# Optimization experiments

Measured on AMD Instinct MI355X. Metric: run time of the kernel, lower is better.

The kernel has to match this reference:

```python
import jax, jax.numpy as jnp
import numpy as np

B, S, F, H = 64, 1024, 64, 128


def setup_inputs() -> dict:
    key = jax.random.key(0)
    ks = jax.random.split(key, 12)
    s = 1.0 / np.sqrt(H)
    u = lambda k, shape: jax.random.uniform(k, shape, jnp.float32, -s, s)
    return {
        "x": jax.random.normal(ks[0], (B, S, F), jnp.float32),
        "mu": jax.random.normal(ks[1], (B, 1, F), jnp.float32),
        "W_ih0": u(ks[2], (4 * H, F)),
        "W_hh0": u(ks[3], (4 * H, H)),
        "b_ih0": u(ks[4], (4 * H,)),
        "b_hh0": u(ks[5], (4 * H,)),
        "W_ih1": u(ks[6], (4 * H, H)),
        "W_hh1": u(ks[7], (4 * H, H)),
        "b_ih1": u(ks[8], (4 * H,)),
        "b_hh1": u(ks[9], (4 * H,)),
        "fc_w": u(ks[10], (1, H)),
        "fc_b": u(ks[11], (1,)),
    }


def _cell(x_gates, h, c, Whh, bias):
    # PyTorch LSTM cell: gates ordered i, f, g, o
    g = x_gates + h @ Whh.T + bias
    i, f, gg, o = jnp.split(g, 4, axis=-1)
    c = jax.nn.sigmoid(f) * c + jax.nn.sigmoid(i) * jnp.tanh(gg)
    h = jax.nn.sigmoid(o) * jnp.tanh(c)
    return h, c


def _lstm2(x1, x2, Wih, Whh, bih, bhh):
    # 2-step LSTM layer from zero initial state; returns per-step hidden states
    bias = bih + bhh
    n = x1.shape[0]
    hd = Whh.shape[1]
    h0 = jnp.zeros((n, hd), x1.dtype)
    h1, c1 = _cell(x1 @ Wih.T, h0, h0, Whh, bias)
    h2, _ = _cell(x2 @ Wih.T, h1, c1, Whh, bias)
    return h1, h2


def reference(x, mu, W_ih0, W_hh0, b_ih0, b_hh0, W_ih1, W_hh1, b_ih1, b_hh1, fc_w, fc_b):
    b, s, f = x.shape
    # Every timestep runs an independent 2-step LSTM [x_t, mu] from zero state,
    # so fold (batch, seq) into one big batch of B*S instances.
    x1 = x.reshape(b * s, f)                                   # step-1 inputs
    x2 = jnp.broadcast_to(mu, (b, s, f)).reshape(b * s, f)     # step-2 inputs (mu)
    h1, h2 = _lstm2(x1, x2, W_ih0, W_hh0, b_ih0, b_hh0)        # layer 0
    _, h2 = _lstm2(h1, h2, W_ih1, W_hh1, b_ih1, b_hh1)         # layer 1
    h = jax.nn.relu(h2).reshape(b, s, -1)                      # relu; dropout is identity (eval)
    out = h @ fc_w.T + fc_b                                    # [B, S, 1]
    return out
```

## Files before the change

### kernel.cpp

```cpp
#include <hip/hip_runtime.h>


typedef _Float16 half8 __attribute__((ext_vector_type(8)));
typedef _Float16 half4_t __attribute__((ext_vector_type(4)));
typedef float f32x4 __attribute__((ext_vector_type(4)));

#define L2E  1.4426950408889634f
#define L2E2 2.8853900817779268f

#define WP_WIH0 0
#define WP_WHH0 32768
#define WP_WIH1 98304
#define WP_WHH1 163840
#define WS_BIAS0 458752
#define WS_BIAS1 (458752 + 2048)
#define WS_MUG2  (458752 + 4096)

__global__ void prep_kernel(const float* __restrict__ Wih0,
                            const float* __restrict__ Whh0,
                            const float* __restrict__ Wih1,
                            const float* __restrict__ Whh1,
                            const float* __restrict__ bih0,
                            const float* __restrict__ bhh0,
                            const float* __restrict__ bih1,
                            const float* __restrict__ bhh1,
                            const float* __restrict__ mu,
                            _Float16* __restrict__ Wp,
                            float* __restrict__ bias0f,
                            float* __restrict__ bias1f,
                            float* __restrict__ mu_g2)
{
    int blk = blockIdx.x;
    if (blk >= 113) {
        int o = (blk - 113) * 256 + threadIdx.x;
        int b = o >> 9;
        int n = o & 511;
        float s = bih0[n] + bhh0[n];
        const float* m = mu + b * 64;
        const float* wrow = Wih0 + n * 64;
        #pragma unroll 8
        for (int k = 0; k < 64; ++k) s += m[k] * wrow[k];
        float scale = ((n >> 7) == 2) ? L2E2 : L2E;
        mu_g2[o] = s * scale;
        return;
    }
    if (blk == 112) {
        int i = threadIdx.x;
        float sc_hi = (i < 128) ? L2E2 : L2E;
        bias0f[i]       = (bih0[i]       + bhh0[i])       * L2E;
        bias0f[i + 256] = (bih0[i + 256] + bhh0[i + 256]) * sc_hi;
        bias1f[i]       = (bih1[i]       + bhh1[i])       * L2E;
        bias1f[i + 256] = (bih1[i + 256] + bhh1[i + 256]) * sc_hi;
        return;
    }
    int gidx = blk * 256 + threadIdx.x;
    const float* src; int KC, Kw, local;
    if (gidx < 4096)       { src = Wih0; KC = 2; Kw = 64;  local = gidx; }
    else if (gidx < 12288) { src = Whh0; KC = 4; Kw = 128; local = gidx - 4096; }
    else if (gidx < 20480) { src = Wih1; KC = 4; Kw = 128; local = gidx - 12288; }
    else                   { src = Whh1; KC = 4; Kw = 128; local = gidx - 20480; }
    int lane = local & 63;
    int tmp  = local >> 6;
    int kc   = tmp % KC;
    int nt   = tmp / KC;
    int n  = nt * 16 + (lane & 15);
    int k0 = kc * 32 + (lane >> 4) * 8;
    float scale = ((n >> 7) == 2) ? L2E2 : L2E;
    const float* s = src + n * Kw + k0;
    half8 hv;
    #pragma unroll
    for (int j = 0; j < 8; ++j) hv[j] = (_Float16)(s[j] * scale);
    *(half8*)(Wp + (size_t)gidx * 8) = hv;
}

__device__ __forceinline__ float sig2(float a) {
    return __builtin_amdgcn_rcpf(1.0f + __builtin_amdgcn_exp2f(-a));
}
__device__ __forceinline__ float tanh2(float a) {
    return fmaf(-2.0f, __builtin_amdgcn_rcpf(1.0f + __builtin_amdgcn_exp2f(a)), 1.0f);
}

__device__ __forceinline__ int swz(int row, int col) {
    return (row << 8) + (col ^ ((row & 7) << 4));
}

__device__ __forceinline__ void lds_barrier() {
    asm volatile("s_waitcnt lgkmcnt(0)" ::: "memory");
    __builtin_amdgcn_s_barrier();
    asm volatile("" ::: "memory");
}

__device__ __forceinline__ void load_bq(half8 bq[4], const _Float16* __restrict__ Wq,
                                        int KC, int kc, int w, int lane)
{
    #pragma unroll
    for (int g = 0; g < 4; ++g)
        bq[g] = *(const half8*)(Wq + (((g * 8 + w) * KC + kc) * 64 + lane) * 8);
}

template<int SRC>
__device__ __forceinline__ void load_a(half8 a[4], const char* base, int kc, int c, int q)
{
    #pragma unroll
    for (int mt = 0; mt < 4; ++mt) {
        if (SRC == 0)
            a[mt] = *(const half8*)((const _Float16*)base + (mt * 16 + c) * 72 + kc * 32 + q * 8);
        else
            a[mt] = *(const half8*)(base + swz(mt * 16 + c, kc * 64 + q * 16));
    }
}

template<int KC, int SRC, bool PF, bool FIRST>
__device__ __forceinline__ void gemm_pf(const _Float16* __restrict__ Wq,
                                        const char* Abase,
                                        const _Float16* __restrict__ Wnext, int KCnext,
                                        half8 bqc[4], const f32x4 bv[4],
                                        int w, int lane, f32x4 acc[4][4])
{
    const int c = lane & 15, q = lane >> 4;
    #pragma unroll
    for (int kc = 0; kc < KC; ++kc) {
        half8 bqn[4];
        if (kc + 1 < KC)  load_bq(bqn, Wq, KC, kc + 1, w, lane);
        else if (PF)      load_bq(bqn, Wnext, KCnext, 0, w, lane);
        half8 a[4];
        load_a<SRC>(a, Abase, kc, c, q);
        __builtin_amdgcn_s_setprio(1);
        #pragma unroll
        for (int mt = 0; mt < 4; ++mt)
            #pragma unroll
            for (int g = 0; g < 4; ++g) {
                f32x4 cin = (FIRST && kc == 0) ? bv[g] : acc[mt][g];
                acc[mt][g] = __builtin_amdgcn_mfma_f32_16x16x32_f16(bqc[g], a[mt], cin, 0, 0, 0);
            }
        __builtin_amdgcn_s_setprio(0);
        if (kc + 1 < KC || PF) {
            #pragma unroll
            for (int g = 0; g < 4; ++g) bqc[g] = bqn[g];
        }
    }
}

__global__ __launch_bounds__(512) void lstm_main(
    const float* __restrict__ x, const _Float16* __restrict__ Wp_in,
    const float* __restrict__ bias0f_in, const float* __restrict__ bias1f_in,
    const float* __restrict__ mu_g2_in, const float* __restrict__ fc_w_in,
    const float* __restrict__ fc_b_in, float* __restrict__ out)
{
    __shared__ __align__(16) char smem[49152];
    char* H1s  = smem;
    char* H2s  = smem + 16384;
    char* H11s = smem + 32768;
    _Float16* A0 = (_Float16*)(smem + 16384);

    const int t = threadIdx.x;
    const int w = t >> 6, lane = t & 63, c = lane & 15, q = lane >> 4;
    const int wg = blockIdx.x;
    const int b = wg >> 4;
    const int bq_idx = w * 4 + q;

    half8 bqc[4];
    load_bq(bqc, Wp_in + WP_WIH0, 2, 0, w, lane);

    {
        const float* xp = x + (size_t)wg * 4096 + t * 8;
        float4 u0 = ((const float4*)xp)[0];
        float4 u1 = ((const float4*)xp)[1];
        half8 hv;
        hv[0] = (_Float16)u0.x; hv[1] = (_Float16)u0.y;
        hv[2] = (_Float16)u0.z; hv[3] = (_Float16)u0.w;
        hv[4] = (_Float16)u1.x; hv[5] = (_Float16)u1.y;
        hv[6] = (_Float16)u1.z; hv[7] = (_Float16)u1.w;
        *(half8*)(A0 + (t >> 3) * 72 + (t & 7) * 8) = hv;
        if (t < 64) out[(size_t)wg * 64 + t] = fc_b_in[0];
    }
    lds_barrier();

    f32x4 acc[4][4];
    float cc[4][4];

    {
        f32x4 bv[4];
        {
            const float* bias0f = bias0f_in; asm volatile("" : "+s"(bias0f));
            #pragma unroll
            for (int g = 0; g < 4; ++g)
                bv[g] = ((const f32x4*)bias0f)[g * 32 + bq_idx];
        }
        gemm_pf<2, 0, true, true>(Wp_in + WP_WIH0, (const char*)A0,
                                  Wp_in + WP_WHH0, 4, bqc, bv, w, lane, acc);
    }
    #pragma unroll
    for (int mt = 0; mt < 4; ++mt) {
        half4_t hv;
        #pragma unroll
        for (int r = 0; r < 4; ++r) {
            float c1 = sig2(acc[mt][0][r]) * tanh2(acc[mt][2][r]);
            cc[mt][r] = c1;
            hv[r] = (_Float16)(sig2(acc[mt][3][r]) * tanh2(c1 * L2E2));
        }
        *(half4_t*)(H1s + swz(mt * 16 + c, w * 32 + q * 8)) = hv;
    }
    lds_barrier();

    {
        f32x4 bv[4];
        {
            const float* mu_g2b = mu_g2_in + b * 512; asm volatile("" : "+s"(mu_g2b));
            #pragma unroll
            for (int g = 0; g < 4; ++g)
                bv[g] = ((const f32x4*)mu_g2b)[g * 32 + bq_idx];
        }
        gemm_pf<4, 1, true, true>(Wp_in + WP_WHH0, H1s,
                                  Wp_in + WP_WIH1, 4, bqc, bv, w, lane, acc);
    }
    #pragma unroll
    for (int mt = 0; mt < 4; ++mt) {
        half4_t hv;
        #pragma unroll
        for (int r = 0; r < 4; ++r) {
            float c2 = sig2(acc[mt][1][r]) * cc[mt][r]
                     + sig2(acc[mt][0][r]) * tanh2(acc[mt][2][r]);
            hv[r] = (_Float16)(sig2(acc[mt][3][r]) * tanh2(c2 * L2E2));
        }
        *(half4_t*)(H2s + swz(mt * 16 + c, w * 32 + q * 8)) = hv;
    }

    {
        f32x4 bv[4];
        {
            const float* bias1f = bias1f_in; asm volatile("" : "+s"(bias1f));
            #pragma unroll
            for (int g = 0; g < 4; ++g)
                bv[g] = ((const f32x4*)bias1f)[g * 32 + bq_idx];
        }
        gemm_pf<4, 1, true, true>(Wp_in + WP_WIH1, H1s,
                                  Wp_in + WP_WIH1, 4, bqc, bv, w, lane, acc);
    }
    #pragma unroll
    for (int mt = 0; mt < 4; ++mt) {
        half4_t hv;
        #pragma unroll
        for (int r = 0; r < 4; ++r) {
            float c1 = sig2(acc[mt][0][r]) * tanh2(acc[mt][2][r]);
            cc[mt][r] = c1;
            hv[r] = (_Float16)(sig2(acc[mt][3][r]) * tanh2(c1 * L2E2));
        }
        *(half4_t*)(H11s + swz(mt * 16 + c, w * 32 + q * 8)) = hv;
    }
    lds_barrier();

    {
        f32x4 bv[4];
        {
            const float* bias1f = bias1f_in; asm volatile("" : "+s"(bias1f));
            #pragma unroll
            for (int g = 0; g < 4; ++g)
                bv[g] = ((const f32x4*)bias1f)[g * 32 + bq_idx];
        }
        gemm_pf<4, 1, true, true>(Wp_in + WP_WIH1, H2s,
                                  Wp_in + WP_WHH1, 4, bqc, bv, w, lane, acc);
    }
    gemm_pf<4, 1, false, false>(Wp_in + WP_WHH1, H11s,
                                nullptr, 0, bqc, nullptr, w, lane, acc);

    {
        const float* fc_w = fc_w_in; asm volatile("" : "+s"(fc_w));
        f32x4 fwv = ((const f32x4*)fc_w)[bq_idx];
        #pragma unroll
        for (int mt = 0; mt < 4; ++mt) {
            float v = 0.0f;
            #pragma unroll
            for (int r = 0; r < 4; ++r) {
                float c2 = sig2(acc[mt][1][r]) * cc[mt][r]
                         + sig2(acc[mt][0][r]) * tanh2(acc[mt][2][r]);
                float h  = sig2(acc[mt][3][r]) * tanh2(c2 * L2E2);
                v = fmaf(fmaxf(h, 0.0f), fwv[r], v);
            }
            v += __shfl_xor(v, 16);
            v += __shfl_xor(v, 32);
            if (lane < 16)
                atomicAdd(out + (size_t)wg * 64 + mt * 16 + lane, v);
        }
    }
}

extern "C" void kernel_launch(void* const* d_in, const int* in_sizes, int n_in,
                              void* d_out, int out_size, void* d_ws, size_t ws_size,
                              hipStream_t stream)
{
    const float* x    = (const float*)d_in[0];
    const float* mu   = (const float*)d_in[1];
    const float* Wih0 = (const float*)d_in[2];
    const float* Whh0 = (const float*)d_in[3];
    const float* bih0 = (const float*)d_in[4];
    const float* bhh0 = (const float*)d_in[5];
    const float* Wih1 = (const float*)d_in[6];
    const float* Whh1 = (const float*)d_in[7];
    const float* bih1 = (const float*)d_in[8];
    const float* bhh1 = (const float*)d_in[9];
    const float* fcw  = (const float*)d_in[10];
    const float* fcb  = (const float*)d_in[11];
    float* out = (float*)d_out;

    _Float16* Wp  = (_Float16*)d_ws;
    float* bias0f = (float*)((char*)d_ws + WS_BIAS0);
    float* bias1f = (float*)((char*)d_ws + WS_BIAS1);
    float* mu_g2  = (float*)((char*)d_ws + WS_MUG2);

    hipLaunchKernelGGL(prep_kernel, dim3(241), dim3(256), 0, stream,
                       Wih0, Whh0, Wih1, Whh1, bih0, bhh0, bih1, bhh1, mu,
                       Wp, bias0f, bias1f, mu_g2);
    hipLaunchKernelGGL(lstm_main, dim3(1024), dim3(512), 0, stream,
                       x, Wp, bias0f, bias1f, mu_g2, fcw, fcb, out);
}
```

Baseline: 133.6 us.

## Process two row tiles per block and skip forget-gate GEMMs at zero state

The grid is halved so each block handles two 64-row tiles in sequence. The second tile's x input is loaded into registers up front, and the final GEMM of tile 0 prefetches the first weights of tile 1, so block launch and weight-load overhead is spread over more work. The forget-gate column block (g==1) is dropped from the first-step GEMMs of both layers, because the initial cell state is zero and that gate's output is never used there. The cost is higher register pressure from the held-over x tile and more template specialisations.

```diff
diff --git a/kernel.cpp b/kernel.cpp
--- a/kernel.cpp
+++ b/kernel.cpp
@@ -90,12 +90,15 @@
     asm volatile("" ::: "memory");
 }
 
+template<bool SKIPF>
 __device__ __forceinline__ void load_bq(half8 bq[4], const _Float16* __restrict__ Wq,
                                         int KC, int kc, int w, int lane)
 {
     #pragma unroll
-    for (int g = 0; g < 4; ++g)
+    for (int g = 0; g < 4; ++g) {
+        if (SKIPF && g == 1) continue;
         bq[g] = *(const half8*)(Wq + (((g * 8 + w) * KC + kc) * 64 + lane) * 8);
+    }
 }
 
 template<int SRC>
@@ -110,7 +113,7 @@
     }
 }
 
-template<int KC, int SRC, bool PF, bool FIRST>
+template<int KC, int SRC, bool PF, bool FIRST, bool SKIPF, bool NSKIPF>
 __device__ __forceinline__ void gemm_pf(const _Float16* __restrict__ Wq,
                                         const char* Abase,
                                         const _Float16* __restrict__ Wnext, int KCnext,
@@ -121,8 +124,8 @@
     #pragma unroll
     for (int kc = 0; kc < KC; ++kc) {
         half8 bqn[4];
-        if (kc + 1 < KC)  load_bq(bqn, Wq, KC, kc + 1, w, lane);
-        else if (PF)      load_bq(bqn, Wnext, KCnext, 0, w, lane);
+        if (kc + 1 < KC)  load_bq<SKIPF>(bqn, Wq, KC, kc + 1, w, lane);
+        else if (PF)      load_bq<NSKIPF>(bqn, Wnext, KCnext, 0, w, lane);
         half8 a[4];
         load_a<SRC>(a, Abase, kc, c, q);
         __builtin_amdgcn_s_setprio(1);
@@ -130,13 +133,19 @@
         for (int mt = 0; mt < 4; ++mt)
             #pragma unroll
             for (int g = 0; g < 4; ++g) {
+                if (SKIPF && g == 1) continue;
                 f32x4 cin = (FIRST && kc == 0) ? bv[g] : acc[mt][g];
                 acc[mt][g] = __builtin_amdgcn_mfma_f32_16x16x32_f16(bqc[g], a[mt], cin, 0, 0, 0);
             }
         __builtin_amdgcn_s_setprio(0);
-        if (kc + 1 < KC || PF) {
-            #pragma unroll
-            for (int g = 0; g < 4; ++g) bqc[g] = bqn[g];
+        if (kc + 1 < KC) {
+            #pragma unroll
+            for (int g = 0; g < 4; ++g)
+                if (!(SKIPF && g == 1)) bqc[g] = bqn[g];
+        } else if (PF) {
+            #pragma unroll
+            for (int g = 0; g < 4; ++g)
+                if (!(NSKIPF && g == 1)) bqc[g] = bqn[g];
         }
     }
 }
@@ -156,14 +165,15 @@
     const int t = threadIdx.x;
     const int w = t >> 6, lane = t & 63, c = lane & 15, q = lane >> 4;
     const int wg = blockIdx.x;
-    const int b = wg >> 4;
+    const int b = wg >> 3;
     const int bq_idx = w * 4 + q;
 
     half8 bqc[4];
-    load_bq(bqc, Wp_in + WP_WIH0, 2, 0, w, lane);
-
+    load_bq<true>(bqc, Wp_in + WP_WIH0, 2, 0, w, lane);
+
+    half8 ax1;
     {
-        const float* xp = x + (size_t)wg * 4096 + t * 8;
+        const float* xp = x + (size_t)wg * 8192 + t * 8;
         float4 u0 = ((const float4*)xp)[0];
         float4 u1 = ((const float4*)xp)[1];
         half8 hv;
@@ -172,115 +182,141 @@
         hv[4] = (_Float16)u1.x; hv[5] = (_Float16)u1.y;
         hv[6] = (_Float16)u1.z; hv[7] = (_Float16)u1.w;
         *(half8*)(A0 + (t >> 3) * 72 + (t & 7) * 8) = hv;
-        if (t < 64) out[(size_t)wg * 64 + t] = fc_b_in[0];
+        const float* xp1 = x + (size_t)wg * 8192 + 4096 + t * 8;
+        float4 v0 = ((const float4*)xp1)[0];
+        float4 v1 = ((const float4*)xp1)[1];
+        ax1[0] = (_Float16)v0.x; ax1[1] = (_Float16)v0.y;
+        ax1[2] = (_Float16)v0.z; ax1[3] = (_Float16)v0.w;
+        ax1[4] = (_Float16)v1.x; ax1[5] = (_Float16)v1.y;
+        ax1[6] = (_Float16)v1.z; ax1[7] = (_Float16)v1.w;
+        if (t < 128) out[(size_t)wg * 128 + t] = fc_b_in[0];
     }
     lds_barrier();
 
     f32x4 acc[4][4];
     float cc[4][4];
 
-    {
-        f32x4 bv[4];
-        {
-            const float* bias0f = bias0f_in; asm volatile("" : "+s"(bias0f));
-            #pragma unroll
-            for (int g = 0; g < 4; ++g)
-                bv[g] = ((const f32x4*)bias0f)[g * 32 + bq_idx];
-        }
-        gemm_pf<2, 0, true, true>(Wp_in + WP_WIH0, (const char*)A0,
-                                  Wp_in + WP_WHH0, 4, bqc, bv, w, lane, acc);
-    }
-    #pragma unroll
-    for (int mt = 0; mt < 4; ++mt) {
-        half4_t hv;
-        #pragma unroll
-        for (int r = 0; r < 4; ++r) {
-            float c1 = sig2(acc[mt][0][r]) * tanh2(acc[mt][2][r]);
-            cc[mt][r] = c1;
-            hv[r] = (_Float16)(sig2(acc[mt][3][r]) * tanh2(c1 * L2E2));
-        }
-        *(half4_t*)(H1s + swz(mt * 16 + c, w * 32 + q * 8)) = hv;
-    }
-    lds_barrier();
-
-    {
-        f32x4 bv[4];
-        {
-            const float* mu_g2b = mu_g2_in + b * 512; asm volatile("" : "+s"(mu_g2b));
-            #pragma unroll
-            for (int g = 0; g < 4; ++g)
-                bv[g] = ((const f32x4*)mu_g2b)[g * 32 + bq_idx];
-        }
-        gemm_pf<4, 1, true, true>(Wp_in + WP_WHH0, H1s,
-                                  Wp_in + WP_WIH1, 4, bqc, bv, w, lane, acc);
-    }
-    #pragma unroll
-    for (int mt = 0; mt < 4; ++mt) {
-        half4_t hv;
-        #pragma unroll
-        for (int r = 0; r < 4; ++r) {
-            float c2 = sig2(acc[mt][1][r]) * cc[mt][r]
-                     + sig2(acc[mt][0][r]) * tanh2(acc[mt][2][r]);
-            hv[r] = (_Float16)(sig2(acc[mt][3][r]) * tanh2(c2 * L2E2));
-        }
-        *(half4_t*)(H2s + swz(mt * 16 + c, w * 32 + q * 8)) = hv;
-    }
-
-    {
-        f32x4 bv[4];
-        {
-            const float* bias1f = bias1f_in; asm volatile("" : "+s"(bias1f));
-            #pragma unroll
-            for (int g = 0; g < 4; ++g)
-                bv[g] = ((const f32x4*)bias1f)[g * 32 + bq_idx];
-        }
-        gemm_pf<4, 1, true, true>(Wp_in + WP_WIH1, H1s,
-                                  Wp_in + WP_WIH1, 4, bqc, bv, w, lane, acc);
-    }
-    #pragma unroll
-    for (int mt = 0; mt < 4; ++mt) {
-        half4_t hv;
-        #pragma unroll
-        for (int r = 0; r < 4; ++r) {
-            float c1 = sig2(acc[mt][0][r]) * tanh2(acc[mt][2][r]);
-            cc[mt][r] = c1;
-            hv[r] = (_Float16)(sig2(acc[mt][3][r]) * tanh2(c1 * L2E2));
-        }
-        *(half4_t*)(H11s + swz(mt * 16 + c, w * 32 + q * 8)) = hv;
-    }
-    lds_barrier();
-
-    {
-        f32x4 bv[4];
-        {
-            const float* bias1f = bias1f_in; asm volatile("" : "+s"(bias1f));
-            #pragma unroll
-            for (int g = 0; g < 4; ++g)
-                bv[g] = ((const f32x4*)bias1f)[g * 32 + bq_idx];
-        }
-        gemm_pf<4, 1, true, true>(Wp_in + WP_WIH1, H2s,
-                                  Wp_in + WP_WHH1, 4, bqc, bv, w, lane, acc);
-    }
-    gemm_pf<4, 1, false, false>(Wp_in + WP_WHH1, H11s,
-                                nullptr, 0, bqc, nullptr, w, lane, acc);
-
-    {
-        const float* fc_w = fc_w_in; asm volatile("" : "+s"(fc_w));
-        f32x4 fwv = ((const f32x4*)fc_w)[bq_idx];
+    #pragma unroll
+    for (int tile = 0; tile < 2; ++tile) {
+        if (tile == 1) lds_barrier();
+
+        {
+            f32x4 bv[4];
+            {
+                const float* bias0f = bias0f_in; asm volatile("" : "+s"(bias0f));
+                #pragma unroll
+                for (int g = 0; g < 4; ++g)
+                    if (g != 1) bv[g] = ((const f32x4*)bias0f)[g * 32 + bq_idx];
+            }
+            gemm_pf<2, 0, true, true, true, false>(
+                Wp_in + WP_WIH0, (const char*)A0,
+                Wp_in + WP_WHH0, 4, bqc, bv, w, lane, acc);
+        }
         #pragma unroll
         for (int mt = 0; mt < 4; ++mt) {
-            float v = 0.0f;
+            half4_t hv;
+            #pragma unroll
+            for (int r = 0; r < 4; ++r) {
+                float c1 = sig2(acc[mt][0][r]) * tanh2(acc[mt][2][r]);
+                cc[mt][r] = c1;
+                hv[r] = (_Float16)(sig2(acc[mt][3][r]) * tanh2(c1 * L2E2));
+            }
+            *(half4_t*)(H1s + swz(mt * 16 + c, w * 32 + q * 8)) = hv;
+        }
+        lds_barrier();
+
+        {
+            f32x4 bv[4];
+            {
+                const float* mu_g2b = mu_g2_in + b * 512; asm volatile("" : "+s"(mu_g2b));
+                #pragma unroll
+                for (int g = 0; g < 4; ++g)
+                    bv[g] = ((const f32x4*)mu_g2b)[g * 32 + bq_idx];
+            }
+            gemm_pf<4, 1, true, true, false, true>(
+                Wp_in + WP_WHH0, H1s,
+                Wp_in + WP_WIH1, 4, bqc, bv, w, lane, acc);
+        }
+        #pragma unroll
+        for (int mt = 0; mt < 4; ++mt) {
+            half4_t hv;
             #pragma unroll
             for (int r = 0; r < 4; ++r) {
                 float c2 = sig2(acc[mt][1][r]) * cc[mt][r]
                          + sig2(acc[mt][0][r]) * tanh2(acc[mt][2][r]);
-                float h  = sig2(acc[mt][3][r]) * tanh2(c2 * L2E2);
-                v = fmaf(fmaxf(h, 0.0f), fwv[r], v);
-            }
-            v += __shfl_xor(v, 16);
-            v += __shfl_xor(v, 32);
-            if (lane < 16)
-                atomicAdd(out + (size_t)wg * 64 + mt * 16 + lane, v);
+                hv[r] = (_Float16)(sig2(acc[mt][3][r]) * tanh2(c2 * L2E2));
+            }
+            *(half4_t*)(H2s + swz(mt * 16 + c, w * 32 + q * 8)) = hv;
+        }
+
+        {
+            f32x4 bv[4];
+            {
+                const float* bias1f = bias1f_in; asm volatile("" : "+s"(bias1f));
+                #pragma unroll
+                for (int g = 0; g < 4; ++g)
+                    if (g != 1) bv[g] = ((const f32x4*)bias1f)[g * 32 + bq_idx];
+            }
+            gemm_pf<4, 1, true, true, true, false>(
+                Wp_in + WP_WIH1, H1s,
+                Wp_in + WP_WIH1, 4, bqc, bv, w, lane, acc);
+        }
+        #pragma unroll
+        for (int mt = 0; mt < 4; ++mt) {
+            half4_t hv;
+            #pragma unroll
+            for (int r = 0; r < 4; ++r) {
+                float c1 = sig2(acc[mt][0][r]) * tanh2(acc[mt][2][r]);
+                cc[mt][r] = c1;
+                hv[r] = (_Float16)(sig2(acc[mt][3][r]) * tanh2(c1 * L2E2));
+            }
+            *(half4_t*)(H11s + swz(mt * 16 + c, w * 32 + q * 8)) = hv;
+        }
+        lds_barrier();
+
+        {
+            f32x4 bv[4];
+            {
+                const float* bias1f = bias1f_in; asm volatile("" : "+s"(bias1f));
+                #pragma unroll
+                for (int g = 0; g < 4; ++g)
+                    bv[g] = ((const f32x4*)bias1f)[g * 32 + bq_idx];
+            }
+            gemm_pf<4, 1, true, true, false, false>(
+                Wp_in + WP_WIH1, H2s,
+                Wp_in + WP_WHH1, 4, bqc, bv, w, lane, acc);
+        }
+
+        if (tile == 0) {
+            lds_barrier();
+            *(half8*)(A0 + (t >> 3) * 72 + (t & 7) * 8) = ax1;
+            gemm_pf<4, 1, true, false, false, true>(
+                Wp_in + WP_WHH1, H11s,
+                Wp_in + WP_WIH0, 2, bqc, nullptr, w, lane, acc);
+        } else {
+            gemm_pf<4, 1, false, false, false, false>(
+                Wp_in + WP_WHH1, H11s,
+                nullptr, 0, bqc, nullptr, w, lane, acc);
+        }
+
+        {
+            const float* fc_w = fc_w_in; asm volatile("" : "+s"(fc_w));
+            f32x4 fwv = ((const f32x4*)fc_w)[bq_idx];
+            #pragma unroll
+            for (int mt = 0; mt < 4; ++mt) {
+                float v = 0.0f;
+                #pragma unroll
+                for (int r = 0; r < 4; ++r) {
+                    float c2 = sig2(acc[mt][1][r]) * cc[mt][r]
+                             + sig2(acc[mt][0][r]) * tanh2(acc[mt][2][r]);
+                    float h  = sig2(acc[mt][3][r]) * tanh2(c2 * L2E2);
+                    v = fmaf(fmaxf(h, 0.0f), fwv[r], v);
+                }
+                v += __shfl_xor(v, 16);
+                v += __shfl_xor(v, 32);
+                if (lane < 16)
+                    atomicAdd(out + (size_t)wg * 128 + tile * 64 + mt * 16 + lane, v);
+            }
         }
     }
 }
@@ -311,6 +347,6 @@
     hipLaunchKernelGGL(prep_kernel, dim3(241), dim3(256), 0, stream,
                        Wih0, Whh0, Wih1, Whh1, bih0, bhh0, bih1, bhh1, mu,
                        Wp, bias0f, bias1f, mu_g2);
-    hipLaunchKernelGGL(lstm_main, dim3(1024), dim3(512), 0, stream,
+    hipLaunchKernelGGL(lstm_main, dim3(512), dim3(512), 0, stream,
                        x, Wp, bias0f, bias1f, mu_g2, fcw, fcb, out);
 }
```

Measured after the change: 136.8 us. 2.3% more time.
